# Optimization experiments

Hardware: AMD Instinct MI355X
Metric: run time of the kernel (lower is better)

Reference implementation:

```python
import jax, jax.numpy as jnp
import numpy as np

FILTER_SIZE = 1024
NUM_HEADS = 16
D_HEAD = FILTER_SIZE // NUM_HEADS
LN_EPS = 1e-5


def setup_inputs() -> dict:
    key = jax.random.key(0)
    ks = jax.random.split(key, 10)
    B, T, D = 2, 2048, FILTER_SIZE
    s = 1.0 / np.sqrt(D)
    return {
        "x": jax.random.normal(ks[0], (B, T, D), dtype=jnp.float32),
        "Wq": jax.random.normal(ks[1], (D, D), dtype=jnp.float32) * s,
        "bq": jnp.zeros((D,), dtype=jnp.float32),
        "Wk": jax.random.normal(ks[2], (D, D), dtype=jnp.float32) * s,
        "bk": jnp.zeros((D,), dtype=jnp.float32),
        "Wv": jax.random.normal(ks[3], (D, D), dtype=jnp.float32) * s,
        "bv": jnp.zeros((D,), dtype=jnp.float32),
        "Wo": jax.random.normal(ks[4], (D, D), dtype=jnp.float32) * s,
        "bo": jnp.zeros((D,), dtype=jnp.float32),
        "gamma": jnp.ones((D,), dtype=jnp.float32),
        "beta": jnp.zeros((D,), dtype=jnp.float32),
    }


def reference(x, Wq, bq, Wk, bk, Wv, bv, Wo, bo, gamma, beta):
    B, T, D = x.shape
    H, Dh = NUM_HEADS, D_HEAD
    # Note: source splits features as (d_head, heads) with heads LAST.
    q = (x @ Wq.T + bq).reshape(B, T, Dh, H)
    k = (x @ Wk.T + bk).reshape(B, T, Dh, H)
    v = (x @ Wv.T + bv).reshape(B, T, Dh, H)
    scale = 1.0 / np.sqrt(Dh).astype(np.float32)
    # scores: (B, H, T, T)
    scores = jnp.einsum("bidh,bjdh->bhij", q, k) * scale
    attn = jax.nn.softmax(scores, axis=-1)  # dropout is identity in eval
    out = jnp.einsum("bhij,bjdh->bidh", attn, v)  # (B, T, Dh, H)
    out = out.reshape(B, T, D)  # matches permute(0,2,3,1).reshape in torch
    out = out @ Wo.T + bo
    out = out + x
    mu = jnp.mean(out, axis=-1, keepdims=True)
    var = jnp.var(out, axis=-1, keepdims=True)
    out = (out - mu) * jax.lax.rsqrt(var + LN_EPS) * gamma + beta
    return out
```

## Files before the change

### kernel.cpp

```cpp
#include <hip/hip_runtime.h>
#include <stdint.h>

#define T_SEQ 2048
#define D_MODEL 1024
#define NH 16
#define DH 64
#define NROWS 4096

typedef __bf16 bf16x8 __attribute__((ext_vector_type(8)));
typedef float floatx4 __attribute__((ext_vector_type(4)));
typedef short short4v __attribute__((ext_vector_type(4)));
typedef short short8v __attribute__((ext_vector_type(8)));

#define AS1 __attribute__((address_space(1)))
#define AS3 __attribute__((address_space(3)))

static __device__ __forceinline__ void gl2lds16(const unsigned short* g, unsigned short* s) {
    __builtin_amdgcn_global_load_lds((const AS1 unsigned int*)g, (AS3 unsigned int*)s, 16, 0, 0);
}

static __device__ __forceinline__ unsigned short f32_bf16(float f) {
    union { float f; unsigned int u; } c; c.f = f;
    unsigned int u = c.u;
    u = u + 0x7FFFu + ((u >> 16) & 1u);
    return (unsigned short)(u >> 16);
}

static __device__ __forceinline__ unsigned int pack2_bf16(float a, float b) {
    return (unsigned int)f32_bf16(a) | ((unsigned int)f32_bf16(b) << 16);
}

static __device__ __forceinline__ floatx4 mfma16(bf16x8 a, bf16x8 b, floatx4 c) {
    return __builtin_amdgcn_mfma_f32_16x16x32_bf16(a, b, c, 0, 0, 0);
}

static __device__ __forceinline__ bf16x8 as_bf(short8v s) {
    union { short8v s; bf16x8 b; } u; u.s = s; return u.b;
}

#define QSCALE 0.1803368801111204f
#define EXP2_SHIFT 10.0f
#define WAITCNT_VM(n) (0x0F70 | (n))

__global__ __launch_bounds__(256) void k_conv_all(const float* __restrict__ x,
                                                  const float* __restrict__ Wq,
                                                  const float* __restrict__ Wk,
                                                  const float* __restrict__ Wv,
                                                  const float* __restrict__ Wo,
                                                  unsigned short* __restrict__ x_bf,
                                                  unsigned short* __restrict__ wqkv_bf,
                                                  unsigned short* __restrict__ wo_bf) {
    __shared__ unsigned short lt[1024];
    int b = blockIdx.x, t = threadIdx.x;
    if (b < 4096) {
        int i = b * 1024 + t * 4;
        float4 v = *(const float4*)(x + i);
        uint2 o;
        o.x = pack2_bf16(v.x, v.y);
        o.y = pack2_bf16(v.z, v.w);
        *(uint2*)(x_bf + i) = o;
    } else if (b < 7168) {
        int idx = b - 4096;
        int tensor = idx >> 10, np = idx & 1023;
        const float* src = tensor == 0 ? Wq : tensor == 1 ? Wk : Wv;
        int f = (np & 63) * 16 + (np >> 6);
        int c = t * 4;
        float4 v = *(const float4*)(src + (long)f * D_MODEL + c);
        uint2 o;
        o.x = pack2_bf16(v.x, v.y);
        o.y = pack2_bf16(v.z, v.w);
        *(uint2*)(wqkv_bf + ((long)tensor * D_MODEL + np) * D_MODEL + c) = o;
    } else {
        int n = b - 7168;
        const float* row = Wo + (long)n * D_MODEL;
        float4 v = *(const float4*)(row + t * 4);
        {
            int f = t * 4;
            lt[((f + 0) & 15) * 64 + ((f + 0) >> 4)] = f32_bf16(v.x);
            lt[((f + 1) & 15) * 64 + ((f + 1) >> 4)] = f32_bf16(v.y);
            lt[((f + 2) & 15) * 64 + ((f + 2) >> 4)] = f32_bf16(v.z);
            lt[((f + 3) & 15) * 64 + ((f + 3) >> 4)] = f32_bf16(v.w);
        }
        __syncthreads();
        *(uint2*)(wo_bf + (long)n * D_MODEL + t * 4) = *(const uint2*)(lt + t * 4);
    }
}

__global__ __launch_bounds__(512, 2) void k_qkv256(const unsigned short* __restrict__ A,
                                                   const unsigned short* __restrict__ W,
                                                   const float* __restrict__ bq,
                                                   const float* __restrict__ bk,
                                                   const float* __restrict__ bv,
                                                   unsigned short* __restrict__ out_bf,
                                                   unsigned short* __restrict__ vtg) {
    __shared__ unsigned short lds[2 * 28672];
    const int tid = threadIdx.x;
    const int w = tid >> 6, l = tid & 63;
    const int lrow = l & 15, lq = l >> 4;
    const int sw8 = lrow & 7;
    const int wm_id = w >> 2, wn_id = w & 3;
    const int L = blockIdx.x;
    const int bx = (L & 7) * 2 + ((L >> 3) & 1);
    const int by = L >> 4;
    const long am0 = (long)bx * 256;
    const long wn0 = (long)by * 192;

    const int rl = l >> 3;
    const int gl = ((l & 7) ^ rl) * 8;

    floatx4 acc[8][3] = {};

    auto stage_piece = [&](int ki, int sel, int piece) {
        int k0 = ki * 64;
        if (piece < 4) {
            int chunk = piece * 8 + w;
            gl2lds16(A + (am0 + chunk * 8 + rl) * D_MODEL + k0 + gl,
                     lds + sel * 28672 + chunk * 512);
        } else {
            int chunk = (piece - 4) * 8 + w;
            gl2lds16(W + (wn0 + chunk * 8 + rl) * D_MODEL + k0 + gl,
                     lds + sel * 28672 + 16384 + chunk * 512);
        }
    };

    #pragma unroll
    for (int pc = 0; pc < 7; pc++) stage_piece(0, 0, pc);
    __builtin_amdgcn_s_waitcnt(WAITCNT_VM(0));
    __builtin_amdgcn_s_barrier();

    for (int t = 0; t < 16; t++) {
        const int sel = t & 1;
        const unsigned short* Ab = lds + sel * 28672;
        const unsigned short* Bb = Ab + 16384;
        if (t < 15) {
            #pragma unroll
            for (int pc = 0; pc < 7; pc++) stage_piece(t + 1, sel ^ 1, pc);
        }
        bf16x8 bfr[3];
        #pragma unroll
        for (int q = 0; q < 4; q++) {
            const int ks = q >> 1, mh = q & 1;
            if (mh == 0) {
                #pragma unroll
                for (int nt = 0; nt < 3; nt++) {
                    int row = wn_id * 48 + nt * 16 + lrow;
                    bfr[nt] = *(const bf16x8*)(Bb + row * 64 + (((ks * 4 + lq) ^ sw8) * 8));
                }
            }
            bf16x8 af[4];
            #pragma unroll
            for (int j = 0; j < 4; j++) {
                int row = wm_id * 128 + (mh * 4 + j) * 16 + lrow;
                af[j] = *(const bf16x8*)(Ab + row * 64 + (((ks * 4 + lq) ^ sw8) * 8));
            }
            __builtin_amdgcn_s_setprio(1);
            #pragma unroll
            for (int j = 0; j < 4; j++)
                #pragma unroll
                for (int nt = 0; nt < 3; nt++)
                    acc[mh * 4 + j][nt] = mfma16(af[j], bfr[nt], acc[mh * 4 + j][nt]);
            __builtin_amdgcn_s_setprio(0);
        }
        __builtin_amdgcn_s_waitcnt(WAITCNT_VM(0));
        __builtin_amdgcn_s_barrier();
    }

    unsigned short* et = lds;
    int row0 = (int)am0 + wm_id * 128;
    int bb_ = row0 >> 11;
    int blkb = (row0 & 2047) >> 6;
    #pragma unroll
    for (int nt = 0; nt < 3; nt++) {
        int n_local = wn_id * 48 + nt * 16 + lrow;
        int n = (int)wn0 + n_local;
        int tensor = n >> 10;
        int np = n & 1023;
        int h = np >> 6, d = np & 63;
        const float* bias = tensor == 0 ? bq : tensor == 1 ? bk : bv;
        float bbv = bias[d * 16 + h];
        float scale = tensor == 0 ? QSCALE : 1.0f;
        if (tensor < 2) {
            #pragma unroll
            for (int mt = 0; mt < 8; mt++) {
                #pragma unroll
                for (int r = 0; r < 4; r++) {
                    int il = wm_id * 128 + mt * 16 + lq * 4 + r;
                    et[il * 200 + n_local] = f32_bf16((acc[mt][nt][r] + bbv) * scale);
                }
            }
        } else {
            #pragma unroll
            for (int mt = 0; mt < 8; mt++) {
                int blk = blkb + (mt >> 2);
                int m4 = mt & 3;
                long base = (((long)(bb_ * 16 + h) * 64 + d) * 32 + blk) * 64;
                uint2 o;
                o.x = pack2_bf16(acc[mt][nt][0] + bbv, acc[mt][nt][1] + bbv);
                o.y = pack2_bf16(acc[mt][nt][2] + bbv, acc[mt][nt][3] + bbv);
                *(uint2*)(vtg + base + (m4 >> 1) * 32 + lq * 8 + (m4 & 1) * 4) = o;
            }
        }
    }
    __syncthreads();
    #pragma unroll
    for (int k = 0; k < 12; k++) {
        int idx = tid + k * 512;
        int il = idx / 24, c = idx % 24;
        int n = (int)wn0 + c * 8;
        int tensor = n >> 10;
        if (tensor < 2) {
            int np = n & 1023;
            int h = np >> 6, d0 = np & 63;
            int row = (int)am0 + il;
            int b = row >> 11, i = row & 2047;
            unsigned short* outt = out_bf + (size_t)tensor * (32u * T_SEQ * DH);
            *(uint4*)(outt + ((long)(b * 16 + h) * T_SEQ + i) * DH + d0) =
                *(const uint4*)(et + il * 200 + c * 8);
        }
    }
}

template <int BN, int MODE>
__global__ __launch_bounds__(256) void k_gemm(const unsigned short* __restrict__ A,
                                              const unsigned short* __restrict__ W,
                                              const float* __restrict__ b0,
                                              const float* __restrict__ resid,
                                              float* __restrict__ out_f32) {
    constexpr int NT = BN / 32;
    constexpr int NCB = BN / 32;
    __shared__ unsigned short lds_a[3 * 128 * 64];
    __shared__ unsigned short lds_b[3 * BN * 64];
    const int tid = threadIdx.x;
    const int w = tid >> 6, l = tid & 63;
    const int lrow = l & 15, lq = l >> 4;
    const int wm = (w >> 1) * 64, wn = (w & 1) * (BN / 2);
    const int L = blockIdx.x;
    const int bx = (L & 7) * 4 + ((L >> 3) & 3);
    const int by = L >> 5;
    const long am0 = (long)bx * 128;
    const long wn0 = (long)by * BN;

    floatx4 acc[4][NT] = {};
    const int grow = l >> 3;
    const int gcol = ((l & 7) ^ grow) * 8;
    const int sw8 = (lrow & 7);

    auto stage = [&](int ki, int sel) {
        unsigned short* la = lds_a + sel * 8192;
        unsigned short* lb = lds_b + sel * (BN * 64);
        int k0 = ki * 64;
        #pragma unroll
        for (int c = 0; c < 4; c++) {
            int chunk = w * 4 + c;
            gl2lds16(A + (am0 + chunk * 8 + grow) * D_MODEL + k0 + gcol, la + chunk * 512);
        }
        #pragma unroll
        for (int c = 0; c < NCB; c++) {
            int chunk = w * NCB + c;
            gl2lds16(W + (wn0 + chunk * 8 + grow) * D_MODEL + k0 + gcol, lb + chunk * 512);
        }
    };

    auto compute = [&](const unsigned short* la, const unsigned short* lb) {
        bf16x8 af[4][2], bfr[NT][2];
        #pragma unroll
        for (int mt = 0; mt < 4; mt++)
            #pragma unroll
            for (int ks = 0; ks < 2; ks++)
                af[mt][ks] = *(const bf16x8*)(la + (wm + mt * 16 + lrow) * 64 +
                                              (((ks * 4 + lq) ^ sw8) * 8));
        #pragma unroll
        for (int nt = 0; nt < NT; nt++)
            #pragma unroll
            for (int ks = 0; ks < 2; ks++)
                bfr[nt][ks] = *(const bf16x8*)(lb + (wn + nt * 16 + lrow) * 64 +
                                               (((ks * 4 + lq) ^ sw8) * 8));
        #pragma unroll
        for (int mt = 0; mt < 4; mt++)
            #pragma unroll
            for (int nt = 0; nt < NT; nt++)
                #pragma unroll
                for (int ks = 0; ks < 2; ks++)
                    acc[mt][nt] = mfma16(af[mt][ks], bfr[nt][ks], acc[mt][nt]);
    };

    stage(0, 0);
    stage(1, 1);
    for (int i = 0; i < 16; i++) {
        const int sel = i % 3;
        if (i < 14) {
            stage(i + 2, (i + 2) % 3);
            __builtin_amdgcn_s_waitcnt(WAITCNT_VM(12));
        } else if (i == 14) {
            __builtin_amdgcn_s_waitcnt(WAITCNT_VM(6));
        } else {
            __builtin_amdgcn_s_waitcnt(WAITCNT_VM(0));
        }
        __builtin_amdgcn_s_barrier();
        compute(lds_a + sel * 8192, lds_b + sel * (BN * 64));
        __builtin_amdgcn_s_barrier();
    }

    #pragma unroll
    for (int mt = 0; mt < 4; mt++) {
        #pragma unroll
        for (int nt = 0; nt < NT; nt++) {
            int n = (int)wn0 + wn + nt * 16 + lrow;
            float bb = b0[n];
            #pragma unroll
            for (int r = 0; r < 4; r++) {
                int row = (int)am0 + wm + mt * 16 + lq * 4 + r;
                long idx = (long)row * D_MODEL + n;
                out_f32[idx] = acc[mt][nt][r] + bb + resid[idx];
            }
        }
    }
}

__global__ __launch_bounds__(256) void k_attn(const unsigned short* __restrict__ q_ws,
                                              const unsigned short* __restrict__ k_ws,
                                              const unsigned short* __restrict__ vtg,
                                              unsigned short* __restrict__ att) {
    __shared__ unsigned short kbuf[4 * 4096];
    __shared__ unsigned short vbuf[4 * 4096];
    const int tid = threadIdx.x;
    const int w = tid >> 6, l = tid & 63;
    const int lrow = l & 15, lq = l >> 4;
    const int sw = lrow & 7;
    const int L = blockIdx.x;
    const int bh = (L & 7) * 4 + ((L >> 3) & 3);
    const int i0 = (L >> 5) * 128;
    const unsigned short* kh = k_ws + (long)bh * T_SEQ * DH;
    const unsigned short* vh = vtg + (long)bh * 64 * T_SEQ;

    const int rl = l >> 3;
    const int gl = ((l & 7) ^ rl) * 8;

    bf16x8 qf[2][2];
    #pragma unroll
    for (int qt = 0; qt < 2; qt++) {
        const unsigned short* qp =
            q_ws + ((long)bh * T_SEQ + i0 + w * 32 + qt * 16 + lrow) * DH + lq * 8;
        qf[qt][0] = *(const bf16x8*)qp;
        qf[qt][1] = *(const bf16x8*)(qp + 32);
    }
    floatx4 o_acc[2][4] = {};
    floatx4 l_acc[2] = {};
    const short8v ones8s = {0x3F80, 0x3F80, 0x3F80, 0x3F80, 0x3F80, 0x3F80, 0x3F80, 0x3F80};
    const bf16x8 ones8 = as_bf(ones8s);

    auto stage = [&](int jt, int sel) {
        unsigned short* kd = kbuf + sel * 4096 + (w * 2) * 512;
        unsigned short* vd = vbuf + sel * 4096 + (w * 2) * 512;
        #pragma unroll
        for (int c = 0; c < 2; c++) {
            int row = w * 16 + c * 8 + rl;
            gl2lds16(kh + ((long)(jt * 64 + row)) * 64 + gl, kd + c * 512);
        }
        #pragma unroll
        for (int c = 0; c < 2; c++) {
            int row = w * 16 + c * 8 + rl;
            gl2lds16(vh + ((long)row * 32 + jt) * 64 + gl, vd + c * 512);
        }
    };

    auto sp4 = [&](floatx4 s) -> short4v {
        float p0 = __builtin_amdgcn_exp2f(s[0]);
        float p1 = __builtin_amdgcn_exp2f(s[1]);
        float p2 = __builtin_amdgcn_exp2f(s[2]);
        float p3 = __builtin_amdgcn_exp2f(s[3]);
        uint2 pk;
        pk.x = __builtin_amdgcn_perm(__float_as_uint(p1), __float_as_uint(p0), 0x07060302);
        pk.y = __builtin_amdgcn_perm(__float_as_uint(p3), __float_as_uint(p2), 0x07060302);
        union { uint2 u; short4v s4; } cv; cv.u = pk;
        return cv.s4;
    };

    auto pv_dt = [&](const unsigned short* vb_, int dt,
                     short8v (&p0)[2], short8v (&p1)[2]) {
        const unsigned short* vp = vb_ + (dt * 16 + lrow) * 64;
        bf16x8 vg0 = *(const bf16x8*)(vp + ((lq ^ sw) * 8));
        bf16x8 vg1 = *(const bf16x8*)(vp + (((4 + lq) ^ sw) * 8));
        o_acc[0][dt] = mfma16(vg0, as_bf(p0[0]), o_acc[0][dt]);
        o_acc[0][dt] = mfma16(vg1, as_bf(p0[1]), o_acc[0][dt]);
        o_acc[1][dt] = mfma16(vg0, as_bf(p1[0]), o_acc[1][dt]);
        o_acc[1][dt] = mfma16(vg1, as_bf(p1[1]), o_acc[1][dt]);
    };

    stage(0, 0);
    stage(1, 1);

    for (int t = 0; t < 32; t++) {
        const int sl = t & 3;
        if (t < 30) stage(t + 2, (t + 2) & 3);
        if (t < 30)
            __builtin_amdgcn_s_waitcnt(WAITCNT_VM(8));
        else if (t == 30)
            __builtin_amdgcn_s_waitcnt(WAITCNT_VM(4));
        else
            __builtin_amdgcn_s_waitcnt(WAITCNT_VM(0));
        __builtin_amdgcn_s_barrier();

        const unsigned short* kb_ = kbuf + sl * 4096;
        const unsigned short* vb_ = vbuf + sl * 4096;

        floatx4 s0[4], s1[4];
        short4v u0[4], u1[4];
        #pragma unroll
        for (int nt = 0; nt < 4; nt++) {
            const unsigned short* kp = kb_ + (nt * 16 + lrow) * 64;
            bf16x8 ka = *(const bf16x8*)(kp + ((lq ^ sw) * 8));
            bf16x8 kb2 = *(const bf16x8*)(kp + (((lq + 4) ^ sw) * 8));
            floatx4 c0 = {-EXP2_SHIFT, -EXP2_SHIFT, -EXP2_SHIFT, -EXP2_SHIFT};
            floatx4 c1 = c0;
            c0 = mfma16(ka, qf[0][0], c0);
            c0 = mfma16(kb2, qf[0][1], c0);
            c1 = mfma16(ka, qf[1][0], c1);
            c1 = mfma16(kb2, qf[1][1], c1);
            s0[nt] = c0;
            s1[nt] = c1;
            if (nt > 0) {
                u0[nt - 1] = sp4(s0[nt - 1]);
                u1[nt - 1] = sp4(s1[nt - 1]);
            }
        }
        u0[3] = sp4(s0[3]);
        u1[3] = sp4(s1[3]);
        short8v pf0[2], pf1[2];
        pf0[0] = __builtin_shufflevector(u0[0], u0[1], 0, 1, 2, 3, 4, 5, 6, 7);
        pf0[1] = __builtin_shufflevector(u0[2], u0[3], 0, 1, 2, 3, 4, 5, 6, 7);
        pf1[0] = __builtin_shufflevector(u1[0], u1[1], 0, 1, 2, 3, 4, 5, 6, 7);
        pf1[1] = __builtin_shufflevector(u1[2], u1[3], 0, 1, 2, 3, 4, 5, 6, 7);
        __builtin_amdgcn_s_setprio(1);
        l_acc[0] = mfma16(ones8, as_bf(pf0[0]), l_acc[0]);
        l_acc[0] = mfma16(ones8, as_bf(pf0[1]), l_acc[0]);
        l_acc[1] = mfma16(ones8, as_bf(pf1[0]), l_acc[1]);
        l_acc[1] = mfma16(ones8, as_bf(pf1[1]), l_acc[1]);
        #pragma unroll
        for (int dt = 0; dt < 4; dt++) pv_dt(vb_, dt, pf0, pf1);
        __builtin_amdgcn_s_setprio(0);
    }

    int h = bh & 15, b = bh >> 4;
    #pragma unroll
    for (int qt = 0; qt < 2; qt++) {
        float rl2 = 1.0f / l_acc[qt][0];
        int i = i0 + w * 32 + qt * 16 + lrow;
        unsigned short* orow = att + ((long)(b * T_SEQ + i)) * D_MODEL + h * 64;
        #pragma unroll
        for (int dt = 0; dt < 4; dt++) {
            uint2 o;
            o.x = pack2_bf16(o_acc[qt][dt][0] * rl2, o_acc[qt][dt][1] * rl2);
            o.y = pack2_bf16(o_acc[qt][dt][2] * rl2, o_acc[qt][dt][3] * rl2);
            *(uint2*)(orow + dt * 16 + lq * 4) = o;
        }
    }
}

__global__ __launch_bounds__(256) void k_ln(float* __restrict__ io,
                                            const float* __restrict__ gamma,
                                            const float* __restrict__ beta) {
    int row = blockIdx.x, t = threadIdx.x;
    float* p = io + (long)row * D_MODEL + t * 4;
    float4 v = *(float4*)p;
    float s = v.x + v.y + v.z + v.w;
    float ss = v.x * v.x + v.y * v.y + v.z * v.z + v.w * v.w;
    #pragma unroll
    for (int m = 1; m < 64; m <<= 1) {
        s += __shfl_xor(s, m);
        ss += __shfl_xor(ss, m);
    }
    __shared__ float red[8];
    if ((t & 63) == 0) { red[t >> 6] = s; red[4 + (t >> 6)] = ss; }
    __syncthreads();
    s = red[0] + red[1] + red[2] + red[3];
    ss = red[4] + red[5] + red[6] + red[7];
    float mu = s * (1.0f / 1024.0f);
    float var = ss * (1.0f / 1024.0f) - mu * mu;
    float rstd = rsqrtf(var + 1e-5f);
    float4 g = *(const float4*)(gamma + t * 4);
    float4 be = *(const float4*)(beta + t * 4);
    float4 o;
    o.x = (v.x - mu) * rstd * g.x + be.x;
    o.y = (v.y - mu) * rstd * g.y + be.y;
    o.z = (v.z - mu) * rstd * g.z + be.z;
    o.w = (v.w - mu) * rstd * g.w + be.w;
    *(float4*)p = o;
}

extern "C" void kernel_launch(void* const* d_in, const int* in_sizes, int n_in,
                              void* d_out, int out_size, void* d_ws, size_t ws_size,
                              hipStream_t stream) {
    const float* x = (const float*)d_in[0];
    const float* Wq = (const float*)d_in[1];
    const float* bq = (const float*)d_in[2];
    const float* Wk = (const float*)d_in[3];
    const float* bk = (const float*)d_in[4];
    const float* Wv = (const float*)d_in[5];
    const float* bv = (const float*)d_in[6];
    const float* Wo = (const float*)d_in[7];
    const float* bo = (const float*)d_in[8];
    const float* gamma = (const float*)d_in[9];
    const float* beta = (const float*)d_in[10];
    float* out = (float*)d_out;

    char* ws = (char*)d_ws;
    unsigned short* x_bf = (unsigned short*)(ws);
    unsigned short* wqkv_bf = (unsigned short*)(ws + ((size_t)8 << 20));
    unsigned short* wo_bf = (unsigned short*)(ws + ((size_t)14 << 20));
    unsigned short* qkv_ws = (unsigned short*)(ws + ((size_t)16 << 20));
    unsigned short* att = x_bf;

    unsigned short* q_ws = qkv_ws;
    unsigned short* k_ws = qkv_ws + (size_t)32 * T_SEQ * DH;
    unsigned short* vtg = qkv_ws + (size_t)64 * T_SEQ * DH;

    k_conv_all<<<8192, 256, 0, stream>>>(x, Wq, Wk, Wv, Wo, x_bf, wqkv_bf, wo_bf);

    k_qkv256<<<256, 512, 0, stream>>>(x_bf, wqkv_bf, bq, bk, bv, qkv_ws, vtg);

    k_attn<<<512, 256, 0, stream>>>(q_ws, k_ws, vtg, att);

    k_gemm<64, 1><<<512, 256, 0, stream>>>(
        att, wo_bf, bo, x, out);

    k_ln<<<NROWS, 256, 0, stream>>>(out, gamma, beta);
}
```

Baseline: 182.9 us.

## Halve attention query tile per block and use triple-buffered K/V staging

The attention kernel now gives each wave 16 query rows instead of 32, so the grid doubles from 512 to 1024 blocks. LDS staging drops from four buffers to three, and the prefetch is issued after the barrier, which changes the wait counts. The aim is more blocks and waves in flight, with less LDS and fewer registers per block, to better fill the GPU. In exchange, every K/V tile is loaded from global memory twice as often relative to the compute done on it, and there is less MFMA work per barrier.

```diff
diff --git a/kernel.cpp b/kernel.cpp
--- a/kernel.cpp
+++ b/kernel.cpp
@@ -321,31 +321,30 @@
                                               const unsigned short* __restrict__ k_ws,
                                               const unsigned short* __restrict__ vtg,
                                               unsigned short* __restrict__ att) {
-    __shared__ unsigned short kbuf[4 * 4096];
-    __shared__ unsigned short vbuf[4 * 4096];
+    __shared__ unsigned short kbuf[3 * 4096];
+    __shared__ unsigned short vbuf[3 * 4096];
     const int tid = threadIdx.x;
     const int w = tid >> 6, l = tid & 63;
     const int lrow = l & 15, lq = l >> 4;
     const int sw = lrow & 7;
     const int L = blockIdx.x;
     const int bh = (L & 7) * 4 + ((L >> 3) & 3);
-    const int i0 = (L >> 5) * 128;
+    const int i0 = (L >> 5) * 64;
     const unsigned short* kh = k_ws + (long)bh * T_SEQ * DH;
     const unsigned short* vh = vtg + (long)bh * 64 * T_SEQ;
 
     const int rl = l >> 3;
     const int gl = ((l & 7) ^ rl) * 8;
 
-    bf16x8 qf[2][2];
-    #pragma unroll
-    for (int qt = 0; qt < 2; qt++) {
+    bf16x8 qf[2];
+    {
         const unsigned short* qp =
-            q_ws + ((long)bh * T_SEQ + i0 + w * 32 + qt * 16 + lrow) * DH + lq * 8;
-        qf[qt][0] = *(const bf16x8*)qp;
-        qf[qt][1] = *(const bf16x8*)(qp + 32);
-    }
-    floatx4 o_acc[2][4] = {};
-    floatx4 l_acc[2] = {};
+            q_ws + ((long)bh * T_SEQ + i0 + w * 16 + lrow) * DH + lq * 8;
+        qf[0] = *(const bf16x8*)qp;
+        qf[1] = *(const bf16x8*)(qp + 32);
+    }
+    floatx4 o_acc[4] = {};
+    floatx4 l_acc = {};
     const short8v ones8s = {0x3F80, 0x3F80, 0x3F80, 0x3F80, 0x3F80, 0x3F80, 0x3F80, 0x3F80};
     const bf16x8 ones8 = as_bf(ones8s);
 
@@ -376,82 +375,62 @@
         return cv.s4;
     };
 
-    auto pv_dt = [&](const unsigned short* vb_, int dt,
-                     short8v (&p0)[2], short8v (&p1)[2]) {
-        const unsigned short* vp = vb_ + (dt * 16 + lrow) * 64;
-        bf16x8 vg0 = *(const bf16x8*)(vp + ((lq ^ sw) * 8));
-        bf16x8 vg1 = *(const bf16x8*)(vp + (((4 + lq) ^ sw) * 8));
-        o_acc[0][dt] = mfma16(vg0, as_bf(p0[0]), o_acc[0][dt]);
-        o_acc[0][dt] = mfma16(vg1, as_bf(p0[1]), o_acc[0][dt]);
-        o_acc[1][dt] = mfma16(vg0, as_bf(p1[0]), o_acc[1][dt]);
-        o_acc[1][dt] = mfma16(vg1, as_bf(p1[1]), o_acc[1][dt]);
-    };
-
     stage(0, 0);
     stage(1, 1);
 
     for (int t = 0; t < 32; t++) {
-        const int sl = t & 3;
-        if (t < 30) stage(t + 2, (t + 2) & 3);
-        if (t < 30)
-            __builtin_amdgcn_s_waitcnt(WAITCNT_VM(8));
-        else if (t == 30)
+        const int sl = t % 3;
+        if (t < 31)
             __builtin_amdgcn_s_waitcnt(WAITCNT_VM(4));
         else
             __builtin_amdgcn_s_waitcnt(WAITCNT_VM(0));
         __builtin_amdgcn_s_barrier();
+        if (t < 30) stage(t + 2, (t + 2) % 3);
 
         const unsigned short* kb_ = kbuf + sl * 4096;
         const unsigned short* vb_ = vbuf + sl * 4096;
 
-        floatx4 s0[4], s1[4];
-        short4v u0[4], u1[4];
+        floatx4 s0[4];
+        short4v u0[4];
         #pragma unroll
         for (int nt = 0; nt < 4; nt++) {
             const unsigned short* kp = kb_ + (nt * 16 + lrow) * 64;
             bf16x8 ka = *(const bf16x8*)(kp + ((lq ^ sw) * 8));
             bf16x8 kb2 = *(const bf16x8*)(kp + (((lq + 4) ^ sw) * 8));
             floatx4 c0 = {-EXP2_SHIFT, -EXP2_SHIFT, -EXP2_SHIFT, -EXP2_SHIFT};
-            floatx4 c1 = c0;
-            c0 = mfma16(ka, qf[0][0], c0);
-            c0 = mfma16(kb2, qf[0][1], c0);
-            c1 = mfma16(ka, qf[1][0], c1);
-            c1 = mfma16(kb2, qf[1][1], c1);
+            c0 = mfma16(ka, qf[0], c0);
+            c0 = mfma16(kb2, qf[1], c0);
             s0[nt] = c0;
-            s1[nt] = c1;
-            if (nt > 0) {
-                u0[nt - 1] = sp4(s0[nt - 1]);
-                u1[nt - 1] = sp4(s1[nt - 1]);
-            }
+            if (nt > 0) u0[nt - 1] = sp4(s0[nt - 1]);
         }
         u0[3] = sp4(s0[3]);
-        u1[3] = sp4(s1[3]);
-        short8v pf0[2], pf1[2];
+        short8v pf0[2];
         pf0[0] = __builtin_shufflevector(u0[0], u0[1], 0, 1, 2, 3, 4, 5, 6, 7);
         pf0[1] = __builtin_shufflevector(u0[2], u0[3], 0, 1, 2, 3, 4, 5, 6, 7);
-        pf1[0] = __builtin_shufflevector(u1[0], u1[1], 0, 1, 2, 3, 4, 5, 6, 7);
-        pf1[1] = __builtin_shufflevector(u1[2], u1[3], 0, 1, 2, 3, 4, 5, 6, 7);
         __builtin_amdgcn_s_setprio(1);
-        l_acc[0] = mfma16(ones8, as_bf(pf0[0]), l_acc[0]);
-        l_acc[0] = mfma16(ones8, as_bf(pf0[1]), l_acc[0]);
-        l_acc[1] = mfma16(ones8, as_bf(pf1[0]), l_acc[1]);
-        l_acc[1] = mfma16(ones8, as_bf(pf1[1]), l_acc[1]);
-        #pragma unroll
-        for (int dt = 0; dt < 4; dt++) pv_dt(vb_, dt, pf0, pf1);
+        l_acc = mfma16(ones8, as_bf(pf0[0]), l_acc);
+        l_acc = mfma16(ones8, as_bf(pf0[1]), l_acc);
+        #pragma unroll
+        for (int dt = 0; dt < 4; dt++) {
+            const unsigned short* vp = vb_ + (dt * 16 + lrow) * 64;
+            bf16x8 vg0 = *(const bf16x8*)(vp + ((lq ^ sw) * 8));
+            bf16x8 vg1 = *(const bf16x8*)(vp + (((4 + lq) ^ sw) * 8));
+            o_acc[dt] = mfma16(vg0, as_bf(pf0[0]), o_acc[dt]);
+            o_acc[dt] = mfma16(vg1, as_bf(pf0[1]), o_acc[dt]);
+        }
         __builtin_amdgcn_s_setprio(0);
     }
 
     int h = bh & 15, b = bh >> 4;
-    #pragma unroll
-    for (int qt = 0; qt < 2; qt++) {
-        float rl2 = 1.0f / l_acc[qt][0];
-        int i = i0 + w * 32 + qt * 16 + lrow;
+    {
+        float rl2 = 1.0f / l_acc[0];
+        int i = i0 + w * 16 + lrow;
         unsigned short* orow = att + ((long)(b * T_SEQ + i)) * D_MODEL + h * 64;
         #pragma unroll
         for (int dt = 0; dt < 4; dt++) {
             uint2 o;
-            o.x = pack2_bf16(o_acc[qt][dt][0] * rl2, o_acc[qt][dt][1] * rl2);
-            o.y = pack2_bf16(o_acc[qt][dt][2] * rl2, o_acc[qt][dt][3] * rl2);
+            o.x = pack2_bf16(o_acc[dt][0] * rl2, o_acc[dt][1] * rl2);
+            o.y = pack2_bf16(o_acc[dt][2] * rl2, o_acc[dt][3] * rl2);
             *(uint2*)(orow + dt * 16 + lq * 4) = o;
         }
     }
@@ -519,7 +498,7 @@
 
     k_qkv256<<<256, 512, 0, stream>>>(x_bf, wqkv_bf, bq, bk, bv, qkv_ws, vtg);
 
-    k_attn<<<512, 256, 0, stream>>>(q_ws, k_ws, vtg, att);
+    k_attn<<<1024, 256, 0, stream>>>(q_ws, k_ws, vtg, att);
 
     k_gemm<64, 1><<<512, 256, 0, stream>>>(
         att, wo_bf, bo, x, out);
```

Result: slower. 199.6 us (+9.2%).
